# Kernel optimization log

Measured on AMD Instinct MI355X. Metric: run time of the kernel, lower is better.

Reference implementation:

```python
import jax, jax.numpy as jnp
import numpy as np

EMB = 768
HEADS = 12
HEAD_DIM = EMB // HEADS
SCALE = HEAD_DIM ** -0.5


def setup_inputs() -> dict:
    key = jax.random.key(0)
    kq, kk, kv, kw = jax.random.split(key, 4)
    B, H, N, D = 2, HEADS, 2048, HEAD_DIM
    queries = jax.random.normal(kq, (B, H, N, D), dtype=jnp.float32)
    keys = jax.random.normal(kk, (B, H, N, D), dtype=jnp.float32)
    values = jax.random.normal(kv, (B, H, N, D), dtype=jnp.float32)
    proj_w = jax.random.normal(kw, (EMB, EMB), dtype=jnp.float32) * (EMB ** -0.5)
    proj_b = jnp.zeros((EMB,), dtype=jnp.float32)
    return {"queries": queries, "keys": keys, "values": values,
            "proj_w": proj_w, "proj_b": proj_b}


def reference(queries, keys, values, proj_w, proj_b):
    # energy: [b, h, n, n] -- full quadratic score matrix, as in the original
    energy = jnp.einsum('bhij,bhkj->bhik', queries, keys) * SCALE
    att = jax.nn.softmax(energy, axis=-1)  # att_drop_p=0.0 -> identity
    out = jnp.einsum('bhij,bhjk->bhik', att, values)  # [b, h, n, d]
    b, h, n, d = out.shape
    out = jnp.transpose(out, (0, 2, 1, 3)).reshape(b, n, h * d)  # 'b h n d -> b n (h d)'
    # nn.Linear: x @ W^T + b (projection dropout is inference identity)
    return out @ proj_w.T + proj_b
```

## Files before the change

### kernel.cpp

```cpp
#include <hip/hip_runtime.h>
#include <cstdint>

typedef short bf16x8 __attribute__((ext_vector_type(8)));
typedef float f32x4 __attribute__((ext_vector_type(4)));
typedef uint16_t u16x4 __attribute__((ext_vector_type(4)));

#define MFMA_16x16x32(a, b, c) __builtin_amdgcn_mfma_f32_16x16x32_bf16((a), (b), (c), 0, 0, 0)

static constexpr int BATCH = 2;
static constexpr int HEADS = 12;
static constexpr int NCTX  = 2048;
static constexpr int DH    = 64;
static constexpr int EMB   = 768;

static constexpr float QSCALE = 0.125f * 1.44269504088896340736f;

__device__ __forceinline__ uint16_t f2bf(float x) {
    uint32_t u = __float_as_uint(x);
    u += 0x7FFFu + ((u >> 16) & 1u);
    return (uint16_t)(u >> 16);
}
__device__ __forceinline__ uint32_t cvt_pk_bf16(float lo, float hi) {
    uint32_t r;
    asm("v_cvt_pk_bf16_f32 %0, %1, %2" : "=v"(r) : "v"(lo), "v"(hi));
    return r;
}

__global__ void k_cvt2(const float* __restrict__ a, uint16_t* __restrict__ da, int n4a,
                       const float* __restrict__ b2, uint16_t* __restrict__ db, int n4b) {
    int i = blockIdx.x * blockDim.x + threadIdx.x;
    const float* src; uint16_t* dst; int j;
    if (i < n4a) { src = a; dst = da; j = i; }
    else {
        j = i - n4a;
        if (j >= n4b) return;
        src = b2; dst = db;
    }
    float4 v = reinterpret_cast<const float4*>(src)[j];
    u16x4 hv = {f2bf(v.x), f2bf(v.y), f2bf(v.z), f2bf(v.w)};
    reinterpret_cast<u16x4*>(dst)[j] = hv;
}

__global__ __launch_bounds__(256) void k_vt(const float* __restrict__ v,
                                            uint16_t* __restrict__ vt) {
    const int bh = blockIdx.y;
    const int n0 = blockIdx.x * 64;
    const int t  = threadIdx.x;
    __shared__ uint16_t tileT[64][72];

    const int r  = t >> 2;
    const int cc = (t & 3) * 16;
    const float* vp = v + ((size_t)bh * NCTX + n0 + r) * DH + cc;
#pragma unroll
    for (int u = 0; u < 4; ++u) {
        float4 x = reinterpret_cast<const float4*>(vp)[u];
        tileT[cc + 4 * u + 0][r] = f2bf(x.x);
        tileT[cc + 4 * u + 1][r] = f2bf(x.y);
        tileT[cc + 4 * u + 2][r] = f2bf(x.z);
        tileT[cc + 4 * u + 3][r] = f2bf(x.w);
    }
    __syncthreads();
    const int d  = t >> 2;
    const int nc = (t & 3) * 16;
    uint16_t* op = vt + ((size_t)bh * DH + d) * NCTX + n0 + nc;
#pragma unroll
    for (int u = 0; u < 2; ++u) {
        bf16x8 x = *reinterpret_cast<const bf16x8*>(&tileT[d][nc + 8 * u]);
        *reinterpret_cast<bf16x8*>(op + 8 * u) = x;
    }
}

__global__ __launch_bounds__(256) void k_attn(
        const float* __restrict__ q, const uint16_t* __restrict__ kb,
        const uint16_t* __restrict__ vt, uint16_t* __restrict__ xb) {
    const int bh = blockIdx.y;
    const int b  = bh / HEADS;
    const int h  = bh % HEADS;
    const int tid = threadIdx.x;
    const int w = tid >> 6;
    const int l = tid & 63;
    const int g = l >> 4;
    const int c = l & 15;

    __shared__ uint16_t K_s[2][64][72];
    __shared__ uint16_t V_s[2][64][72];
    __shared__ uint16_t P_s[4][16][72];

    const int q0 = blockIdx.x * 64 + w * 16;

    bf16x8 qa[2];
    {
        const float* qp = q + ((size_t)bh * NCTX + q0 + c) * DH + 8 * g;
#pragma unroll
        for (int kf = 0; kf < 2; ++kf) {
            float4 x0 = *reinterpret_cast<const float4*>(qp + kf * 32);
            float4 x1 = *reinterpret_cast<const float4*>(qp + kf * 32 + 4);
            bf16x8 f;
            f[0] = (short)f2bf(x0.x * QSCALE); f[1] = (short)f2bf(x0.y * QSCALE);
            f[2] = (short)f2bf(x0.z * QSCALE); f[3] = (short)f2bf(x0.w * QSCALE);
            f[4] = (short)f2bf(x1.x * QSCALE); f[5] = (short)f2bf(x1.y * QSCALE);
            f[6] = (short)f2bf(x1.z * QSCALE); f[7] = (short)f2bf(x1.w * QSCALE);
            qa[kf] = f;
        }
    }

    f32x4 zero = {0.f, 0.f, 0.f, 0.f};
    f32x4 o[4] = {zero, zero, zero, zero};
    float m = -1e30f;
    float lsum = 0.f;

    const int srow = tid >> 3;
    const int sch  = tid & 7;

    const uint16_t* kb_b = kb + (size_t)bh * NCTX * DH + srow * DH + sch * 8;
    const uint16_t* vt_b = vt + (size_t)bh * DH * NCTX + srow * NCTX + sch * 8;

    {
        bf16x8 a0 = *reinterpret_cast<const bf16x8*>(kb_b);
        bf16x8 a1 = *reinterpret_cast<const bf16x8*>(kb_b + 32 * DH);
        bf16x8 v0 = *reinterpret_cast<const bf16x8*>(vt_b);
        bf16x8 v1 = *reinterpret_cast<const bf16x8*>(vt_b + 32 * NCTX);
        *reinterpret_cast<bf16x8*>(&K_s[0][srow][sch * 8])      = a0;
        *reinterpret_cast<bf16x8*>(&K_s[0][srow + 32][sch * 8]) = a1;
        *reinterpret_cast<bf16x8*>(&V_s[0][srow][sch * 8])      = v0;
        *reinterpret_cast<bf16x8*>(&V_s[0][srow + 32][sch * 8]) = v1;
    }
    __syncthreads();

    for (int t = 0; t < NCTX / 64; ++t) {
        const int cur = t & 1;
        const int nxt = cur ^ 1;

        bf16x8 nk0, nk1, nv0, nv1;
        const bool pf = (t + 1) < NCTX / 64;
        if (pf) {
            const size_t ko = (size_t)(t + 1) * 64 * DH;
            const size_t vo = (size_t)(t + 1) * 64;
            nk0 = *reinterpret_cast<const bf16x8*>(kb_b + ko);
            nk1 = *reinterpret_cast<const bf16x8*>(kb_b + ko + 32 * DH);
            nv0 = *reinterpret_cast<const bf16x8*>(vt_b + vo);
            nv1 = *reinterpret_cast<const bf16x8*>(vt_b + vo + 32 * NCTX);
        }

        f32x4 s[4] = {zero, zero, zero, zero};
        __builtin_amdgcn_s_setprio(1);
#pragma unroll
        for (int nf = 0; nf < 4; ++nf) {
#pragma unroll
            for (int kf = 0; kf < 2; ++kf) {
                bf16x8 bhf = *reinterpret_cast<const bf16x8*>(&K_s[cur][nf * 16 + c][kf * 32 + 8 * g]);
                s[nf] = MFMA_16x16x32(bhf, qa[kf], s[nf]);
            }
        }
        __builtin_amdgcn_s_setprio(0);

        float pm0 = fmaxf(fmaxf(s[0][0], s[0][1]), fmaxf(s[0][2], s[0][3]));
        float pm1 = fmaxf(fmaxf(s[1][0], s[1][1]), fmaxf(s[1][2], s[1][3]));
        float pm2 = fmaxf(fmaxf(s[2][0], s[2][1]), fmaxf(s[2][2], s[2][3]));
        float pm3 = fmaxf(fmaxf(s[3][0], s[3][1]), fmaxf(s[3][2], s[3][3]));
        float pmax = fmaxf(fmaxf(pm0, pm1), fmaxf(pm2, pm3));

        if (!__all(pmax <= m + 11.0f)) {
            float smax = fmaxf(pmax, __shfl_xor(pmax, 16));
            smax = fmaxf(smax, __shfl_xor(smax, 32));
            float mnew = fmaxf(m, smax);
            float corr = __builtin_amdgcn_exp2f(m - mnew);
            m = mnew;
            lsum *= corr;
#pragma unroll
            for (int r = 0; r < 4; ++r) {
                float cr = __shfl(corr, 4 * g + r);
#pragma unroll
                for (int f = 0; f < 4; ++f) o[f][r] *= cr;
            }
        }

#pragma unroll
        for (int nf = 0; nf < 4; ++nf) {
            float p0 = __builtin_amdgcn_exp2f(s[nf][0] - m);
            float p1 = __builtin_amdgcn_exp2f(s[nf][1] - m);
            float p2 = __builtin_amdgcn_exp2f(s[nf][2] - m);
            float p3 = __builtin_amdgcn_exp2f(s[nf][3] - m);
            lsum += (p0 + p1) + (p2 + p3);
            uint2 pk;
            pk.x = cvt_pk_bf16(p0, p1);
            pk.y = cvt_pk_bf16(p2, p3);
            *reinterpret_cast<uint2*>(&P_s[w][c][16 * nf + 4 * g]) = pk;
        }

        bf16x8 pa0 = *reinterpret_cast<const bf16x8*>(&P_s[w][c][8 * g]);
        bf16x8 pa1 = *reinterpret_cast<const bf16x8*>(&P_s[w][c][32 + 8 * g]);
        __builtin_amdgcn_s_setprio(1);
#pragma unroll
        for (int f = 0; f < 4; ++f) {
            bf16x8 b0 = *reinterpret_cast<const bf16x8*>(&V_s[cur][f * 16 + c][8 * g]);
            bf16x8 b1 = *reinterpret_cast<const bf16x8*>(&V_s[cur][f * 16 + c][32 + 8 * g]);
            o[f] = MFMA_16x16x32(pa0, b0, o[f]);
            o[f] = MFMA_16x16x32(pa1, b1, o[f]);
        }
        __builtin_amdgcn_s_setprio(0);

        if (pf) {
            *reinterpret_cast<bf16x8*>(&K_s[nxt][srow][sch * 8])      = nk0;
            *reinterpret_cast<bf16x8*>(&K_s[nxt][srow + 32][sch * 8]) = nk1;
            *reinterpret_cast<bf16x8*>(&V_s[nxt][srow][sch * 8])      = nv0;
            *reinterpret_cast<bf16x8*>(&V_s[nxt][srow + 32][sch * 8]) = nv1;
        }
        __syncthreads();
    }

    lsum += __shfl_xor(lsum, 16);
    lsum += __shfl_xor(lsum, 32);
    const float linv = 1.0f / lsum;

    const size_t xbase = ((size_t)b * NCTX + q0) * EMB + h * DH;
#pragma unroll
    for (int r = 0; r < 4; ++r) {
        float lr = __shfl(linv, 4 * g + r);
#pragma unroll
        for (int f = 0; f < 4; ++f) {
            float v = o[f][r] * lr;
            size_t addr = xbase + (size_t)(4 * g + r) * EMB + f * 16 + c;
            xb[addr] = f2bf(v);
        }
    }
}

__global__ __launch_bounds__(256) void k_proj(
        const uint16_t* __restrict__ xb, const uint16_t* __restrict__ wb,
        const float* __restrict__ bias, float* __restrict__ out) {
    const int tid = threadIdx.x;
    const int w = tid >> 6;
    const int l = tid & 63;
    const int g = l >> 4;
    const int c = l & 15;
    const int m0 = blockIdx.x * 64 + w * 16;
    const int n0 = blockIdx.y * 64;

    __shared__ uint16_t W_s[64][72];

    f32x4 zero = {0.f, 0.f, 0.f, 0.f};
    f32x4 acc[4] = {zero, zero, zero, zero};

    const int srow = tid >> 2;
    const int sch  = tid & 3;
    constexpr int ROUNDS = EMB / 64;

    const uint16_t* whp = wb + (size_t)(n0 + srow) * EMB + sch * 8;
    const uint16_t* xhp = xb + (size_t)(m0 + c) * EMB + 8 * g;

    bf16x8 w0 = *reinterpret_cast<const bf16x8*>(whp);
    bf16x8 w1 = *reinterpret_cast<const bf16x8*>(whp + 32);
    bf16x8 a0 = *reinterpret_cast<const bf16x8*>(xhp);
    bf16x8 a1 = *reinterpret_cast<const bf16x8*>(xhp + 32);

    for (int rd = 0; rd < ROUNDS; ++rd) {
        __syncthreads();
        *reinterpret_cast<bf16x8*>(&W_s[srow][sch * 8])      = w0;
        *reinterpret_cast<bf16x8*>(&W_s[srow][32 + sch * 8]) = w1;
        __syncthreads();

        const int rn = (rd + 1 < ROUNDS) ? (rd + 1) : (ROUNDS - 1);
        bf16x8 w0n = *reinterpret_cast<const bf16x8*>(whp + (size_t)rn * 64);
        bf16x8 w1n = *reinterpret_cast<const bf16x8*>(whp + (size_t)rn * 64 + 32);
        bf16x8 a0n = *reinterpret_cast<const bf16x8*>(xhp + (size_t)rn * 64);
        bf16x8 a1n = *reinterpret_cast<const bf16x8*>(xhp + (size_t)rn * 64 + 32);

        __builtin_amdgcn_s_setprio(1);
#pragma unroll
        for (int nf = 0; nf < 4; ++nf) {
            bf16x8 b0 = *reinterpret_cast<const bf16x8*>(&W_s[nf * 16 + c][8 * g]);
            bf16x8 b1 = *reinterpret_cast<const bf16x8*>(&W_s[nf * 16 + c][32 + 8 * g]);
            acc[nf] = MFMA_16x16x32(a0, b0, acc[nf]);
            acc[nf] = MFMA_16x16x32(a1, b1, acc[nf]);
        }
        __builtin_amdgcn_s_setprio(0);

        w0 = w0n; w1 = w1n; a0 = a0n; a1 = a1n;
    }

#pragma unroll
    for (int nf = 0; nf < 4; ++nf) {
#pragma unroll
        for (int r = 0; r < 4; ++r) {
            int row = m0 + g * 4 + r;
            int col = n0 + nf * 16 + c;
            out[(size_t)row * EMB + col] = acc[nf][r] + bias[col];
        }
    }
}

extern "C" void kernel_launch(void* const* d_in, const int* in_sizes, int n_in,
                              void* d_out, int out_size, void* d_ws, size_t ws_size,
                              hipStream_t stream) {
    const float* q    = (const float*)d_in[0];
    const float* k    = (const float*)d_in[1];
    const float* v    = (const float*)d_in[2];
    const float* pw   = (const float*)d_in[3];
    const float* pb   = (const float*)d_in[4];
    float* out = (float*)d_out;

    const size_t nqkv = (size_t)BATCH * HEADS * NCTX * DH;
    const size_t nx   = (size_t)BATCH * NCTX * EMB;
    const size_t nw   = (size_t)EMB * EMB;

    uint8_t* ws = (uint8_t*)d_ws;
    uint16_t* kb = (uint16_t*)ws;              ws += nqkv * 2;
    uint16_t* vt = (uint16_t*)ws;              ws += nqkv * 2;
    uint16_t* xb = (uint16_t*)ws;              ws += nx * 2;
    uint16_t* wb = (uint16_t*)ws;              ws += nw * 2;

    const int n4k = (int)(nqkv / 4);
    const int n4w = (int)(nw / 4);
    k_cvt2<<<(n4k + n4w + 255) / 256, 256, 0, stream>>>(k, kb, n4k, pw, wb, n4w);
    k_vt<<<dim3(NCTX / 64, BATCH * HEADS), 256, 0, stream>>>(v, vt);

    k_attn<<<dim3(NCTX / 64, BATCH * HEADS), 256, 0, stream>>>(q, kb, vt, xb);

    k_proj<<<dim3((BATCH * NCTX) / 64, EMB / 64), 256, 0, stream>>>(xb, wb, pb, out);
}
```

Measured before the change: 78.28 us.

## Pre-swizzle V into MFMA fragment layout and load directly into registers

The V transpose kernel now writes V in an MFMA-fragment-ordered layout, so each lane holds its B operands in 64 contiguous 16-byte chunks per slot. The attention kernel drops the V shared-memory double buffer and loads the eight V fragments per tile straight from global memory into registers. This removes the LDS writes and reads for V and frees shared memory. In exchange, the global V loads are issued in the same iteration they are used, with no software prefetch, so their latency may be exposed.

```diff
diff --git a/kernel.cpp b/kernel.cpp
--- a/kernel.cpp
+++ b/kernel.cpp
@@ -60,19 +60,24 @@
         tileT[cc + 4 * u + 3][r] = f2bf(x.w);
     }
     __syncthreads();
-    const int d  = t >> 2;
-    const int nc = (t & 3) * 16;
-    uint16_t* op = vt + ((size_t)bh * DH + d) * NCTX + n0 + nc;
+
+    const int l2 = t & 63;
+    const int s0 = t >> 6;
+    const int gg = l2 >> 4;
+    const int c2 = l2 & 15;
+    uint16_t* vb = vt + ((size_t)bh * 32 + (n0 >> 6)) * 8 * 512;
 #pragma unroll
     for (int u = 0; u < 2; ++u) {
-        bf16x8 x = *reinterpret_cast<const bf16x8*>(&tileT[d][nc + 8 * u]);
-        *reinterpret_cast<bf16x8*>(op + 8 * u) = x;
+        const int slot = s0 + 4 * u;
+        const int f = slot >> 1, h = slot & 1;
+        bf16x8 x = *reinterpret_cast<const bf16x8*>(&tileT[f * 16 + c2][h * 32 + 8 * gg]);
+        *reinterpret_cast<bf16x8*>(vb + (size_t)slot * 512 + l2 * 8) = x;
     }
 }
 
 __global__ __launch_bounds__(256) void k_attn(
         const float* __restrict__ q, const uint16_t* __restrict__ kb,
-        const uint16_t* __restrict__ vt, uint16_t* __restrict__ xb) {
+        const uint16_t* __restrict__ vf, uint16_t* __restrict__ xb) {
     const int bh = blockIdx.y;
     const int b  = bh / HEADS;
     const int h  = bh % HEADS;
@@ -83,7 +88,6 @@
     const int c = l & 15;
 
     __shared__ uint16_t K_s[2][64][72];
-    __shared__ uint16_t V_s[2][64][72];
     __shared__ uint16_t P_s[4][16][72];
 
     const int q0 = blockIdx.x * 64 + w * 16;
@@ -113,17 +117,13 @@
     const int sch  = tid & 7;
 
     const uint16_t* kb_b = kb + (size_t)bh * NCTX * DH + srow * DH + sch * 8;
-    const uint16_t* vt_b = vt + (size_t)bh * DH * NCTX + srow * NCTX + sch * 8;
+    const uint16_t* vf_b = vf + (size_t)bh * 32 * 8 * 512 + (size_t)l * 8;
 
     {
         bf16x8 a0 = *reinterpret_cast<const bf16x8*>(kb_b);
         bf16x8 a1 = *reinterpret_cast<const bf16x8*>(kb_b + 32 * DH);
-        bf16x8 v0 = *reinterpret_cast<const bf16x8*>(vt_b);
-        bf16x8 v1 = *reinterpret_cast<const bf16x8*>(vt_b + 32 * NCTX);
         *reinterpret_cast<bf16x8*>(&K_s[0][srow][sch * 8])      = a0;
         *reinterpret_cast<bf16x8*>(&K_s[0][srow + 32][sch * 8]) = a1;
-        *reinterpret_cast<bf16x8*>(&V_s[0][srow][sch * 8])      = v0;
-        *reinterpret_cast<bf16x8*>(&V_s[0][srow + 32][sch * 8]) = v1;
     }
     __syncthreads();
 
@@ -131,16 +131,18 @@
         const int cur = t & 1;
         const int nxt = cur ^ 1;
 
-        bf16x8 nk0, nk1, nv0, nv1;
+        bf16x8 nk0, nk1;
         const bool pf = (t + 1) < NCTX / 64;
         if (pf) {
             const size_t ko = (size_t)(t + 1) * 64 * DH;
-            const size_t vo = (size_t)(t + 1) * 64;
             nk0 = *reinterpret_cast<const bf16x8*>(kb_b + ko);
             nk1 = *reinterpret_cast<const bf16x8*>(kb_b + ko + 32 * DH);
-            nv0 = *reinterpret_cast<const bf16x8*>(vt_b + vo);
-            nv1 = *reinterpret_cast<const bf16x8*>(vt_b + vo + 32 * NCTX);
-        }
+        }
+
+        bf16x8 vr[8];
+#pragma unroll
+        for (int s = 0; s < 8; ++s)
+            vr[s] = *reinterpret_cast<const bf16x8*>(vf_b + ((size_t)t * 8 + s) * 512);
 
         f32x4 s[4] = {zero, zero, zero, zero};
         __builtin_amdgcn_s_setprio(1);
@@ -193,18 +195,14 @@
         __builtin_amdgcn_s_setprio(1);
 #pragma unroll
         for (int f = 0; f < 4; ++f) {
-            bf16x8 b0 = *reinterpret_cast<const bf16x8*>(&V_s[cur][f * 16 + c][8 * g]);
-            bf16x8 b1 = *reinterpret_cast<const bf16x8*>(&V_s[cur][f * 16 + c][32 + 8 * g]);
-            o[f] = MFMA_16x16x32(pa0, b0, o[f]);
-            o[f] = MFMA_16x16x32(pa1, b1, o[f]);
+            o[f] = MFMA_16x16x32(pa0, vr[2 * f],     o[f]);
+            o[f] = MFMA_16x16x32(pa1, vr[2 * f + 1], o[f]);
         }
         __builtin_amdgcn_s_setprio(0);
 
         if (pf) {
             *reinterpret_cast<bf16x8*>(&K_s[nxt][srow][sch * 8])      = nk0;
             *reinterpret_cast<bf16x8*>(&K_s[nxt][srow + 32][sch * 8]) = nk1;
-            *reinterpret_cast<bf16x8*>(&V_s[nxt][srow][sch * 8])      = nv0;
-            *reinterpret_cast<bf16x8*>(&V_s[nxt][srow + 32][sch * 8]) = nv1;
         }
         __syncthreads();
     }
@@ -306,16 +304,16 @@
 
     uint8_t* ws = (uint8_t*)d_ws;
     uint16_t* kb = (uint16_t*)ws;              ws += nqkv * 2;
-    uint16_t* vt = (uint16_t*)ws;              ws += nqkv * 2;
+    uint16_t* vf = (uint16_t*)ws;              ws += nqkv * 2;
     uint16_t* xb = (uint16_t*)ws;              ws += nx * 2;
     uint16_t* wb = (uint16_t*)ws;              ws += nw * 2;
 
     const int n4k = (int)(nqkv / 4);
     const int n4w = (int)(nw / 4);
     k_cvt2<<<(n4k + n4w + 255) / 256, 256, 0, stream>>>(k, kb, n4k, pw, wb, n4w);
-    k_vt<<<dim3(NCTX / 64, BATCH * HEADS), 256, 0, stream>>>(v, vt);
-
-    k_attn<<<dim3(NCTX / 64, BATCH * HEADS), 256, 0, stream>>>(q, kb, vt, xb);
+    k_vt<<<dim3(NCTX / 64, BATCH * HEADS), 256, 0, stream>>>(v, vf);
+
+    k_attn<<<dim3(NCTX / 64, BATCH * HEADS), 256, 0, stream>>>(q, kb, vf, xb);
 
     k_proj<<<dim3((BATCH * NCTX) / 64, EMB / 64), 256, 0, stream>>>(xb, wb, pb, out);
 }
```

Result: no change. 77.59 us (-0.9%).
